# Kernel optimization log

Measured on AMD Instinct MI355X. Metric: run time of the kernel, lower is better.

Reference implementation:

```python
import jax, jax.numpy as jnp
import numpy as np

B, N, C, H, W = 2, 1000, 256, 50, 50
P = 7                      # pooled size
NUM_CLASSES = 91
REP = 1024
IMG = 800
SCALE = 1.0 / 16.0         # feature stride
SCORE_THRESH = 0.05
NMS_THRESH = 0.5
DET = 100
BW = (10.0, 10.0, 5.0, 5.0)  # bbox_reg_weights
BBOX_CLIP = float(np.log(1000.0 / 16.0))
NEG = -1e9


def setup_inputs() -> dict:
    key = jax.random.key(0)
    ks = jax.random.split(key, 8)
    features = jax.random.normal(ks[0], (B, C, H, W), jnp.float32)
    # valid proposal boxes inside the image
    xy = jax.random.uniform(ks[1], (B, N, 2), jnp.float32) * (IMG * 0.6)
    wh = jax.random.uniform(ks[2], (B, N, 2), jnp.float32) * (IMG * 0.35) + 8.0
    proposals = jnp.concatenate([xy, jnp.minimum(xy + wh, IMG - 1.0)], axis=-1)
    D_in = C * P * P
    w1 = jax.random.normal(ks[3], (D_in, REP), jnp.float32) / np.sqrt(D_in)
    b1 = jnp.zeros((REP,), jnp.float32)
    w2 = jax.random.normal(ks[4], (REP, REP), jnp.float32) / np.sqrt(REP)
    b2 = jnp.zeros((REP,), jnp.float32)
    w_cls = jax.random.normal(ks[5], (REP, NUM_CLASSES), jnp.float32) / np.sqrt(REP)
    b_cls = jnp.zeros((NUM_CLASSES,), jnp.float32)
    w_bbox = jax.random.normal(ks[6], (REP, NUM_CLASSES * 4), jnp.float32) * 0.001
    b_bbox = jnp.zeros((NUM_CLASSES * 4,), jnp.float32)
    return dict(features=features, proposals=proposals, w1=w1, b1=b1, w2=w2, b2=b2,
                w_cls=w_cls, b_cls=b_cls, w_bbox=w_bbox, b_bbox=b_bbox, image_size=IMG)


def _roi_align(feat, rois):
    """feat [C,H,W], rois [N,4] -> pooled [N,C,P,P] (aligned, 1 sample per bin)."""
    r = rois * SCALE
    x1, y1, x2, y2 = r[:, 0], r[:, 1], r[:, 2], r[:, 3]
    bw = (x2 - x1) / P
    bh = (y2 - y1) / P
    cc = jnp.arange(P, dtype=feat.dtype) + 0.5
    ys = y1[:, None] + cc[None, :] * bh[:, None] - 0.5   # [N,P]
    xs = x1[:, None] + cc[None, :] * bw[:, None] - 0.5   # [N,P]
    y = jnp.clip(jnp.broadcast_to(ys[:, :, None], (ys.shape[0], P, P)), 0.0, H - 1.0)
    x = jnp.clip(jnp.broadcast_to(xs[:, None, :], (xs.shape[0], P, P)), 0.0, W - 1.0)
    y0 = jnp.floor(y).astype(jnp.int32)
    x0 = jnp.floor(x).astype(jnp.int32)
    y1i = jnp.minimum(y0 + 1, H - 1)
    x1i = jnp.minimum(x0 + 1, W - 1)
    ly = y - y0.astype(feat.dtype); lx = x - x0.astype(feat.dtype)
    hy = 1.0 - ly; hx = 1.0 - lx
    # gathers: [C, N, P, P]
    val = (feat[:, y0, x0] * (hy * hx) + feat[:, y0, x1i] * (hy * lx)
           + feat[:, y1i, x0] * (ly * hx) + feat[:, y1i, x1i] * (ly * lx))
    return jnp.transpose(val, (1, 0, 2, 3))


def _decode_clip(bbox, props, img):
    """bbox [B,N,K,4] deltas, props [B,N,4] -> boxes [B,N,K,4] clipped to image."""
    pw = props[..., 2] - props[..., 0]
    ph = props[..., 3] - props[..., 1]
    pcx = props[..., 0] + 0.5 * pw
    pcy = props[..., 1] + 0.5 * ph
    dx = bbox[..., 0] / BW[0]
    dy = bbox[..., 1] / BW[1]
    dw = jnp.minimum(bbox[..., 2] / BW[2], BBOX_CLIP)
    dh = jnp.minimum(bbox[..., 3] / BW[3], BBOX_CLIP)
    cx = dx * pw[..., None] + pcx[..., None]
    cy = dy * ph[..., None] + pcy[..., None]
    w = pw[..., None] * jnp.exp(dw)
    h = ph[..., None] * jnp.exp(dh)
    boxes = jnp.stack([cx - 0.5 * w, cy - 0.5 * h, cx + 0.5 * w, cy + 0.5 * h], axis=-1)
    return jnp.clip(boxes, 0.0, float(img))


def _nms_one(boxes, scores, img):
    """boxes [N,K,4], scores [N,K] (background already dropped) -> dets [DET,5], labels [DET]."""
    K = scores.shape[1]
    labels = jnp.broadcast_to(jnp.arange(1, K + 1), scores.shape).reshape(-1)
    b = boxes.reshape(-1, 4)
    s = scores.reshape(-1)
    wv = b[:, 2] - b[:, 0]
    hv = b[:, 3] - b[:, 1]
    valid = (s > SCORE_THRESH) & (wv >= 1.0) & (hv >= 1.0)  # score thresh + remove_small_boxes
    swork = jnp.where(valid, s, NEG)
    # batched_nms via per-class coordinate offset
    off = labels.astype(b.dtype) * (float(img) + 2.0)
    boff = b + off[:, None]
    areas = (boff[:, 2] - boff[:, 0]) * (boff[:, 3] - boff[:, 1])

    def body(sw, _):
        i = jnp.argmax(sw)
        ok = sw[i] > NEG / 2
        bi = boff[i]
        ix1 = jnp.maximum(bi[0], boff[:, 0]); iy1 = jnp.maximum(bi[1], boff[:, 1])
        ix2 = jnp.minimum(bi[2], boff[:, 2]); iy2 = jnp.minimum(bi[3], boff[:, 3])
        inter = jnp.clip(ix2 - ix1, 0.0) * jnp.clip(iy2 - iy1, 0.0)
        iou = inter / (areas[i] + areas - inter + 1e-9)
        sw = jnp.where((iou > NMS_THRESH) & ok, NEG, sw)
        sw = sw.at[i].set(NEG)
        return sw, (i, ok)

    _, (idx, oks) = jax.lax.scan(body, swork, None, length=DET)
    db = jnp.where(oks[:, None], b[idx], 0.0)
    ds = jnp.where(oks, s[idx], 0.0)
    dl = jnp.where(oks, labels[idx], -1)
    return jnp.concatenate([db, ds[:, None]], axis=-1), dl


def reference(features, proposals, w1, b1, w2, b2, w_cls, b_cls, w_bbox, b_bbox, image_size):
    # box_roi_pool: RoIAlign 7x7 per image
    pooled = jax.vmap(_roi_align)(features, proposals)          # [B,N,C,P,P]
    feats = pooled.reshape(B * N, C * P * P)
    # box_head: TwoMLPHead
    h = jax.nn.relu(feats @ w1 + b1)
    h = jax.nn.relu(h @ w2 + b2)
    # box_predictor
    logits = h @ w_cls + b_cls                                   # [B*N, 91]
    bbox = (h @ w_bbox + b_bbox).reshape(B, N, NUM_CLASSES, 4)
    scores = jax.nn.softmax(logits, axis=-1).reshape(B, N, NUM_CLASSES)
    boxes = _decode_clip(bbox, proposals, image_size)            # [B,N,91,4]
    # drop background class 0, then per-image class-aware NMS
    boxes_k = boxes[:, :, 1:, :]
    scores_k = scores[:, :, 1:]
    dets, labels = jax.vmap(lambda bb, ss: _nms_one(bb, ss, image_size))(boxes_k, scores_k)
    return dets, labels  # dets [B,DET,5] = (x1,y1,x2,y2,score); labels [B,DET]
```

## Files before the change

### kernel.cpp

```cpp
#include <hip/hip_runtime.h>
#include <stdint.h>

#define B_    2
#define N_    1000
#define C_    256
#define H_    50
#define W_    50
#define P_    7
#define NCLS  91
#define REP_  1024
#define DIN   (C_ * P_ * P_)
#define M_    (B_ * N_)
#define MPAD  2048
#define HOUT  512
#define DET_  100
#define NMSM  (N_ * 90)
#define NEGV  (-1000000000.0f)
#define SCALE_ 0.0625f
#define IMGF  800.0f
#define BBOX_CLIPF 4.135166556742356f

#define RC_   25
#define CC_   4

typedef __bf16 bf16_t;
typedef __attribute__((ext_vector_type(8))) __bf16 bf16x8;
typedef __attribute__((ext_vector_type(4))) __bf16 bf16x4;
typedef __attribute__((ext_vector_type(4))) float f32x4;

__device__ __forceinline__ void gload16(const void* g, void* l) {
  auto gp = (const __attribute__((address_space(1))) uint32_t*)(uintptr_t)g;
  auto lp = (__attribute__((address_space(3))) uint32_t*)(uint32_t)(uintptr_t)l;
  __builtin_amdgcn_global_load_lds(gp, lp, 16, 0, 0);
}

__global__ __launch_bounds__(256) void roi_kernel(const float* __restrict__ features,
                                                  const float* __restrict__ proposals,
                                                  bf16_t* __restrict__ A) {
  const int cc0 = blockIdx.x * CC_;
  const int roiBase = blockIdx.y * RC_;
  const int t = threadIdx.x;
  if (roiBase >= M_) {
    for (int idx = t; idx < RC_ * 49; idx += 256) {
      const int r = idx / 49, pp = idx - r * 49;
      const int n = roiBase + r;
      if (n < MPAD) {
        bf16_t* arow = A + (size_t)n * DIN + cc0 * 49 + pp;
#pragma unroll
        for (int c = 0; c < CC_; ++c) arow[c * 49] = (bf16_t)0.0f;
      }
    }
    return;
  }
  __shared__ __align__(16) float s_pl[CC_ * 2500];
  __shared__ float s_ly[RC_ * 49];
  __shared__ float s_lx[RC_ * 49];
  __shared__ unsigned short s_off[RC_ * 49];
  const int b = (roiBase >= N_) ? 1 : 0;
  const f32x4* src = (const f32x4*)(features + (size_t)(b * C_ + cc0) * (H_ * W_));
  f32x4* dst = (f32x4*)s_pl;
  for (int i = t; i < CC_ * 2500 / 4; i += 256) dst[i] = src[i];
  for (int idx = t; idx < RC_ * 49; idx += 256) {
    const int r = idx / 49, pp = idx - r * 49;
    const int py = pp / 7, px = pp - py * 7;
    const float* p = proposals + (roiBase + r) * 4;
    float y1 = p[1] * SCALE_, y2 = p[3] * SCALE_;
    float bh = (y2 - y1) * (1.0f / 7.0f);
    float y = y1 + ((float)py + 0.5f) * bh - 0.5f;
    y = fminf(fmaxf(y, 0.0f), 49.0f);
    int y0 = (int)floorf(y);
    int dy = (y0 < 49) ? 1 : 0;
    float ly = y - (float)y0;
    float x1 = p[0] * SCALE_, x2 = p[2] * SCALE_;
    float bw = (x2 - x1) * (1.0f / 7.0f);
    float x = x1 + ((float)px + 0.5f) * bw - 0.5f;
    x = fminf(fmaxf(x, 0.0f), 49.0f);
    int x0 = (int)floorf(x);
    int dx = (x0 < 49) ? 1 : 0;
    float lx = x - (float)x0;
    s_off[idx] = (unsigned short)((y0 * W_ + x0) | (dx << 12) | (dy << 13));
    s_ly[idx] = ly;
    s_lx[idx] = lx;
  }
  __syncthreads();
  for (int idx = t; idx < RC_ * 49; idx += 256) {
    const int r = idx / 49, pp = idx - r * 49;
    const unsigned off = s_off[idx];
    const float ly = s_ly[idx], lx = s_lx[idx];
    const float hy = 1.0f - ly, hx = 1.0f - lx;
    const int o00 = off & 0xFFF;
    const int dx = (off >> 12) & 1;
    const int o10 = o00 + W_ * ((off >> 13) & 1);
    const float w00 = hy * hx, w01 = hy * lx, w10 = ly * hx, w11 = ly * lx;
    bf16_t* arow = A + (size_t)(roiBase + r) * DIN + cc0 * 49 + pp;
#pragma unroll
    for (int c = 0; c < CC_; ++c) {
      const float* pl = s_pl + c * 2500;
      float v = pl[o00] * w00 + pl[o00 + dx] * w01 + pl[o10] * w10 + pl[o10 + dx] * w11;
      arow[c * 49] = (bf16_t)v;
    }
  }
}

__global__ __launch_bounds__(256) void transpose_kernel(const float* __restrict__ in,
                                                        bf16_t* __restrict__ out,
                                                        int K, int N) {
  __shared__ float tile[32][33];
  const int k0 = blockIdx.x * 32;
  const int n0 = blockIdx.y * 32;
  const int tx = threadIdx.x & 31;
  const int ty = threadIdx.x >> 5;
#pragma unroll
  for (int j = 0; j < 4; ++j) {
    int ky = ty + j * 8;
    tile[ky][tx] = in[(size_t)(k0 + ky) * N + n0 + tx];
  }
  __syncthreads();
  const int qx = threadIdx.x & 7;
  const int ny = threadIdx.x >> 3;
  bf16x4 o;
#pragma unroll
  for (int i = 0; i < 4; ++i) o[i] = (bf16_t)tile[4 * qx + i][ny];
  *(bf16x4*)(&out[(size_t)(n0 + ny) * K + k0 + 4 * qx]) = o;
}

__global__ __launch_bounds__(256) void headw_kernel(const float* __restrict__ wcls,
                                                    const float* __restrict__ wbb,
                                                    bf16_t* __restrict__ wht) {
  int idx = blockIdx.x * 256 + threadIdx.x;
  int j = idx >> 10;
  int k = idx & 1023;
  float v = 0.0f;
  if (j < NCLS) v = wcls[(size_t)k * NCLS + j];
  else if (j < 455) v = wbb[(size_t)k * 364 + (j - NCLS)];
  wht[idx] = (bf16_t)v;
}

__global__ void headb_kernel(const float* __restrict__ bcls,
                             const float* __restrict__ bbb,
                             float* __restrict__ biash) {
  int j = threadIdx.x;
  float v = 0.0f;
  if (j < NCLS) v = bcls[j];
  else if (j < 455) v = bbb[j - NCLS];
  biash[j] = v;
}

__global__ __launch_bounds__(512, 2) void gemm8_kernel(const bf16_t* __restrict__ A,
                                                       const bf16_t* __restrict__ Bt,
                                                       bf16_t* __restrict__ partial,
                                                       int K, int kLen, int KC) {
  __shared__ __align__(16) bf16_t lds[4 * 2 * 2 * 128 * 32];
  const int t = threadIdx.x;
  const int lane = t & 63;
  const int w = t >> 6;
  const int wm = w >> 2;
  const int wn = w & 3;
  const int bid = blockIdx.x;
  const int zc = bid % KC;
  const int inner = bid / KC;
  const int row0 = (inner >> 2) * 256;
  const int col0 = (inner & 3) * 256;
  const int kOff = zc * kLen;
  const int G = kLen >> 5;

  const int lr = lane & 15;
  const int kb = (lane >> 4) * 16;
  int aoff[8], boff[4];
#pragma unroll
  for (int m = 0; m < 8; ++m) {
    int r = m * 16 + lr;
    aoff[m] = (r * 64 + kb) ^ (((r >> 3) & 1) << 5);
  }
#pragma unroll
  for (int n = 0; n < 4; ++n) {
    int r = (wn & 1) * 64 + n * 16 + lr;
    boff[n] = (r * 64 + kb) ^ (((r >> 3) & 1) << 5);
  }

  const int s_row = t >> 2;
  const int s_k8 = (t & 3) ^ (((s_row >> 3) & 1) << 1);
  const bf16_t* pAs = A + (size_t)(row0 + s_row) * K + kOff + s_k8 * 8;
  const bf16_t* pBs = Bt + (size_t)(col0 + s_row) * K + kOff + s_k8 * 8;
  const size_t halfStride = (size_t)128 * K;
  char* ldsBase = (char*)&lds[0];
  const int wOff = w << 10;

  auto stage = [&](int buf, int hp, int kt) {
    const bf16_t* src = ((hp < 2) ? pAs : pBs) + (size_t)(hp & 1) * halfStride + kt * 32;
    char* dst = ldsBase + buf * 32768 + (hp >> 1) * 16384 + (hp & 1) * 8192 + wOff;
    gload16(src, dst);
  };

  f32x4 acc[8][4] = {};

#pragma unroll
  for (int hp = 0; hp < 4; ++hp) stage(0, hp, 0);
#pragma unroll
  for (int hp = 0; hp < 4; ++hp) stage(1, hp, 1);
#pragma unroll
  for (int hp = 0; hp < 4; ++hp) stage(2, hp, 2);
  asm volatile("s_waitcnt vmcnt(8)" ::: "memory");
  __builtin_amdgcn_s_barrier();
  __builtin_amdgcn_sched_barrier(0);

  for (int g = 0; g < G; ++g) {
    const int cb = g & 3;
    const int sb = (g + 3) & 3;
    const bool doStage = (g + 3) < G;
    if (doStage) {
#pragma unroll
      for (int hp = 0; hp < 4; ++hp) stage(sb, hp, g + 3);
    }
    char* lA = ldsBase + cb * 32768 + wm * 8192;
    char* lB = ldsBase + cb * 32768 + 16384 + (wn >> 1) * 8192;
    bf16x8 af[8], bfv[4];
#pragma unroll
    for (int i = 0; i < 8; ++i) af[i] = *(const bf16x8*)(lA + aoff[i]);
#pragma unroll
    for (int j2 = 0; j2 < 4; ++j2) bfv[j2] = *(const bf16x8*)(lB + boff[j2]);
    asm volatile("s_waitcnt lgkmcnt(0)" ::: "memory");
    if (doStage)          asm volatile("s_waitcnt vmcnt(8)" ::: "memory");
    else if (g == G - 3)  asm volatile("s_waitcnt vmcnt(4)" ::: "memory");
    else                  asm volatile("s_waitcnt vmcnt(0)" ::: "memory");
    __builtin_amdgcn_sched_barrier(0);
    __builtin_amdgcn_s_barrier();
    __builtin_amdgcn_sched_barrier(0);
    __builtin_amdgcn_s_setprio(1);
#pragma unroll
    for (int i = 0; i < 8; ++i)
#pragma unroll
      for (int j2 = 0; j2 < 4; ++j2)
        acc[i][j2] = __builtin_amdgcn_mfma_f32_16x16x32_bf16(af[i], bfv[j2], acc[i][j2], 0, 0, 0);
    __builtin_amdgcn_s_setprio(0);
    __builtin_amdgcn_sched_barrier(0);
  }

  bf16_t* out = partial + (size_t)zc * MPAD * REP_;
  const int crow = (lane >> 4) * 4;
#pragma unroll
  for (int n = 0; n < 4; ++n) {
    const int col = col0 + wn * 64 + n * 16 + lr;
#pragma unroll
    for (int m = 0; m < 8; ++m) {
      const int rowb = row0 + wm * 128 + m * 16 + crow;
#pragma unroll
      for (int j2 = 0; j2 < 4; ++j2)
        out[(size_t)(rowb + j2) * REP_ + col] = (bf16_t)acc[m][n][j2];
    }
  }
}

__global__ __launch_bounds__(256) void gemm_kernel(const bf16_t* __restrict__ A,
                                                   const bf16_t* __restrict__ Bt,
                                                   float* __restrict__ partial,
                                                   int K, int ldc, int kLen) {
  __shared__ __align__(16) bf16_t As[128 * 32];
  __shared__ __align__(16) bf16_t Bs[128 * 32];
  const int t = threadIdx.x;
  const int lane = t & 63;
  const int wid = t >> 6;
  const int row0 = blockIdx.x * 128;
  const int col0 = blockIdx.y * 128;
  const int kOff = blockIdx.z * kLen;

  f32x4 acc[4][4] = {};

  const int rA = t >> 2;
  const int sA = t & 3;
  const bf16_t* aSrc1 = A + (size_t)(row0 + rA) * K + sA * 8 + kOff;
  const bf16_t* aSrc2 = A + (size_t)(row0 + rA + 64) * K + sA * 8 + kOff;
  const bf16_t* bSrc1 = Bt + (size_t)(col0 + rA) * K + sA * 8 + kOff;
  const bf16_t* bSrc2 = Bt + (size_t)(col0 + rA + 64) * K + sA * 8 + kOff;
  char* AsB = (char*)&As[0];
  char* BsB = (char*)&Bs[0];
  const int ldsOff1 = (wid * 64) * 16;
  const int ldsOff2 = (wid * 64 + 256) * 16;

  const int wm = wid >> 1;
  const int wn = wid & 1;
  const int lr = lane & 15;
  const int lk16 = (lane >> 4) * 16;
  int aOff[4], bOff[4];
#pragma unroll
  for (int m = 0; m < 4; ++m) aOff[m] = (wm * 64 + m * 16 + lr) * 64 + lk16;
#pragma unroll
  for (int n = 0; n < 4; ++n) bOff[n] = (wn * 64 + n * 16 + lr) * 64 + lk16;

  for (int k0 = 0; k0 < kLen; k0 += 32) {
    gload16(aSrc1 + k0, AsB + ldsOff1);
    gload16(aSrc2 + k0, AsB + ldsOff2);
    gload16(bSrc1 + k0, BsB + ldsOff1);
    gload16(bSrc2 + k0, BsB + ldsOff2);
    __syncthreads();
    bf16x8 af[4], bfv[4];
#pragma unroll
    for (int m = 0; m < 4; ++m) af[m] = *(const bf16x8*)(AsB + aOff[m]);
#pragma unroll
    for (int n = 0; n < 4; ++n) bfv[n] = *(const bf16x8*)(BsB + bOff[n]);
#pragma unroll
    for (int m = 0; m < 4; ++m)
#pragma unroll
      for (int n = 0; n < 4; ++n)
        acc[m][n] = __builtin_amdgcn_mfma_f32_16x16x32_bf16(af[m], bfv[n], acc[m][n], 0, 0, 0);
    __syncthreads();
  }

  float* out = partial + (size_t)blockIdx.z * MPAD * ldc;
  const int crow = (lane >> 4) * 4;
  const int ccol = lane & 15;
#pragma unroll
  for (int n = 0; n < 4; ++n) {
    const int col = col0 + wn * 64 + n * 16 + ccol;
#pragma unroll
    for (int m = 0; m < 4; ++m) {
      const int rowb = row0 + wm * 64 + m * 16 + crow;
#pragma unroll
      for (int j = 0; j < 4; ++j) {
        out[(size_t)(rowb + j) * ldc + col] = acc[m][n][j];
      }
    }
  }
}

__global__ __launch_bounds__(256) void reduceH_kernel(const bf16_t* __restrict__ partial,
                                                      const float* __restrict__ bias,
                                                      bf16_t* __restrict__ out,
                                                      int KC) {
  const size_t idx8 = ((size_t)blockIdx.x * 256 + threadIdx.x) * 8;
  const size_t stride = (size_t)MPAD * REP_;
  float s[8] = {};
  for (int c = 0; c < KC; ++c) {
    const bf16x8 v = *(const bf16x8*)(partial + c * stride + idx8);
#pragma unroll
    for (int j = 0; j < 8; ++j) s[j] += (float)v[j];
  }
  const int col = (int)(idx8 & (size_t)(REP_ - 1));
  const f32x4 b0 = *(const f32x4*)(bias + col);
  const f32x4 b1 = *(const f32x4*)(bias + col + 4);
  bf16x8 o;
#pragma unroll
  for (int j = 0; j < 4; ++j) o[j] = (bf16_t)fmaxf(s[j] + b0[j], 0.0f);
#pragma unroll
  for (int j = 0; j < 4; ++j) o[4 + j] = (bf16_t)fmaxf(s[4 + j] + b1[j], 0.0f);
  *(bf16x8*)(out + idx8) = o;
}

__global__ __launch_bounds__(256) void reduce_kernel(const float* __restrict__ partial,
                                                     const float* __restrict__ bias,
                                                     void* __restrict__ out,
                                                     int ldc, int KC, int mode) {
  const size_t idx4 = ((size_t)blockIdx.x * 256 + threadIdx.x) * 4;
  f32x4 s = *(const f32x4*)(partial + idx4);
  const size_t stride = (size_t)MPAD * ldc;
  for (int c = 1; c < KC; ++c) s += *(const f32x4*)(partial + c * stride + idx4);
  const int col = (int)(idx4 & (size_t)(ldc - 1));
  const f32x4 bv = *(const f32x4*)(bias + col);
  s += bv;
  if (mode) {
    bf16x4 o;
#pragma unroll
    for (int j = 0; j < 4; ++j) o[j] = (bf16_t)fmaxf(s[j], 0.0f);
    *(bf16x4*)((bf16_t*)out + idx4) = o;
  } else {
    *(f32x4*)((float*)out + idx4) = s;
  }
}

__global__ __launch_bounds__(256) void rowsm_kernel(const float* __restrict__ ho,
                                                    float* __restrict__ mxv,
                                                    float* __restrict__ invv) {
  const int row = blockIdx.x * 4 + (threadIdx.x >> 6);
  const int lane = threadIdx.x & 63;
  if (row >= M_) return;
  const float* r = ho + (size_t)row * HOUT;
  float v1 = (lane < NCLS) ? r[lane] : -3.0e38f;
  float v2 = (lane + 64 < NCLS) ? r[lane + 64] : -3.0e38f;
  float mx = fmaxf(v1, v2);
#pragma unroll
  for (int off = 32; off; off >>= 1) mx = fmaxf(mx, __shfl_xor(mx, off));
  float s = ((lane < NCLS) ? expf(v1 - mx) : 0.0f) + ((lane + 64 < NCLS) ? expf(v2 - mx) : 0.0f);
#pragma unroll
  for (int off = 32; off; off >>= 1) s += __shfl_xor(s, off);
  if (lane == 0) { mxv[row] = mx; invv[row] = 1.0f / s; }
}

__global__ __launch_bounds__(256) void decode_kernel(const float* __restrict__ ho,
                                                     const float* __restrict__ mxv,
                                                     const float* __restrict__ invv,
                                                     const float* __restrict__ props,
                                                     float* __restrict__ boxes,
                                                     float* __restrict__ scores,
                                                     float* __restrict__ swork,
                                                     float* __restrict__ boff,
                                                     float* __restrict__ area) {
  const int idx = blockIdx.x * 256 + threadIdx.x;
  if (idx >= M_ * 90) return;
  const int n = idx / 90;
  const int k = idx - n * 90 + 1;
  const float* row = ho + (size_t)n * HOUT;
  const float sc = expf(row[k] - mxv[n]) * invv[n];
  const float* p = props + n * 4;
  const float px1 = p[0], py1 = p[1], px2 = p[2], py2 = p[3];
  const float pw = px2 - px1, ph = py2 - py1;
  const float pcx = px1 + 0.5f * pw, pcy = py1 + 0.5f * ph;
  const float* d = row + NCLS + 4 * k;
  const float dx = d[0] * 0.1f;
  const float dy = d[1] * 0.1f;
  const float dw = fminf(d[2] * 0.2f, BBOX_CLIPF);
  const float dh = fminf(d[3] * 0.2f, BBOX_CLIPF);
  const float cx = dx * pw + pcx, cy = dy * ph + pcy;
  const float w = pw * expf(dw), h = ph * expf(dh);
  const float bx1 = fminf(fmaxf(cx - 0.5f * w, 0.0f), IMGF);
  const float by1 = fminf(fmaxf(cy - 0.5f * h, 0.0f), IMGF);
  const float bx2 = fminf(fmaxf(cx + 0.5f * w, 0.0f), IMGF);
  const float by2 = fminf(fmaxf(cy + 0.5f * h, 0.0f), IMGF);
  const int j = idx;
  boxes[4 * j + 0] = bx1; boxes[4 * j + 1] = by1;
  boxes[4 * j + 2] = bx2; boxes[4 * j + 3] = by2;
  scores[j] = sc;
  const float wv = bx2 - bx1, hv = by2 - by1;
  swork[j] = ((sc > 0.05f) && (wv >= 1.0f) && (hv >= 1.0f)) ? sc : NEGV;
  const float off = (float)k * (IMGF + 2.0f);
  const float ox1 = bx1 + off, oy1 = by1 + off, ox2 = bx2 + off, oy2 = by2 + off;
  boff[4 * j + 0] = ox1; boff[4 * j + 1] = oy1;
  boff[4 * j + 2] = ox2; boff[4 * j + 3] = oy2;
  area[j] = (ox2 - ox1) * (oy2 - oy1);
}

__global__ __launch_bounds__(1024) void nms_kernel(const float* __restrict__ boxes,
                                                   const float* __restrict__ scores,
                                                   float* __restrict__ swork,
                                                   const float* __restrict__ boff,
                                                   const float* __restrict__ area,
                                                   float* __restrict__ dout) {
  const int b = blockIdx.x;
  const int t = threadIdx.x;
  const float* Bx = boxes + (size_t)b * NMSM * 4;
  const float* Sc = scores + (size_t)b * NMSM;
  float* Sw = swork + (size_t)b * NMSM;
  const float* Bo = boff + (size_t)b * NMSM * 4;
  const float* Ar = area + (size_t)b * NMSM;
  float* dets = dout + b * (DET_ * 5);
  float* labels = dout + B_ * DET_ * 5 + b * DET_;
  __shared__ float s_val[1024];
  __shared__ int s_idx[1024];
  __shared__ float s_box[4];
  __shared__ float s_area;
  __shared__ int s_ok;
  for (int it = 0; it < DET_; ++it) {
    float bv = -3.0e38f;
    int bi = 0;
    for (int j = t; j < NMSM; j += 1024) {
      float v = Sw[j];
      if (v > bv) { bv = v; bi = j; }
    }
    s_val[t] = bv;
    s_idx[t] = bi;
    __syncthreads();
    for (int off = 512; off > 0; off >>= 1) {
      if (t < off) {
        float v2 = s_val[t + off]; int i2 = s_idx[t + off];
        if (v2 > s_val[t] || (v2 == s_val[t] && i2 < s_idx[t])) { s_val[t] = v2; s_idx[t] = i2; }
      }
      __syncthreads();
    }
    if (t == 0) {
      int i = s_idx[0];
      int ok = (s_val[0] > NEGV * 0.5f) ? 1 : 0;
      s_ok = ok;
      if (ok) {
        dets[it * 5 + 0] = Bx[i * 4 + 0];
        dets[it * 5 + 1] = Bx[i * 4 + 1];
        dets[it * 5 + 2] = Bx[i * 4 + 2];
        dets[it * 5 + 3] = Bx[i * 4 + 3];
        dets[it * 5 + 4] = Sc[i];
        labels[it] = (float)(i % 90 + 1);
        s_box[0] = Bo[i * 4 + 0]; s_box[1] = Bo[i * 4 + 1];
        s_box[2] = Bo[i * 4 + 2]; s_box[3] = Bo[i * 4 + 3];
        s_area = Ar[i];
        Sw[i] = NEGV;
      }
    }
    __syncthreads();
    if (!s_ok) {
      for (int tt = it + t; tt < DET_; tt += 1024) {
        dets[tt * 5 + 0] = 0.0f; dets[tt * 5 + 1] = 0.0f; dets[tt * 5 + 2] = 0.0f;
        dets[tt * 5 + 3] = 0.0f; dets[tt * 5 + 4] = 0.0f;
        labels[tt] = -1.0f;
      }
      return;
    }
    const float bx1 = s_box[0], by1 = s_box[1], bx2 = s_box[2], by2 = s_box[3], ai = s_area;
    for (int j = t; j < NMSM; j += 1024) {
      float v = Sw[j];
      if (v <= NEGV * 0.5f) continue;
      float ix1 = fmaxf(bx1, Bo[j * 4 + 0]);
      float iy1 = fmaxf(by1, Bo[j * 4 + 1]);
      float ix2 = fminf(bx2, Bo[j * 4 + 2]);
      float iy2 = fminf(by2, Bo[j * 4 + 3]);
      float inter = fmaxf(ix2 - ix1, 0.0f) * fmaxf(iy2 - iy1, 0.0f);
      float iou = inter / (ai + Ar[j] - inter + 1e-9f);
      if (iou > 0.5f) Sw[j] = NEGV;
    }
    __syncthreads();
  }
}

extern "C" void kernel_launch(void* const* d_in, const int* in_sizes, int n_in,
                              void* d_out, int out_size, void* d_ws, size_t ws_size,
                              hipStream_t stream) {
  const float* features  = (const float*)d_in[0];
  const float* proposals = (const float*)d_in[1];
  const float* w1   = (const float*)d_in[2];
  const float* b1   = (const float*)d_in[3];
  const float* w2   = (const float*)d_in[4];
  const float* b2   = (const float*)d_in[5];
  const float* wcls = (const float*)d_in[6];
  const float* bcls = (const float*)d_in[7];
  const float* wbb  = (const float*)d_in[8];
  const float* bbb  = (const float*)d_in[9];
  (void)in_sizes; (void)n_in; (void)out_size;

  char* p = (char*)d_ws;
  auto alloc = [&](size_t bytes) {
    char* r = p;
    p += (bytes + 255) & ~(size_t)255;
    return r;
  };
  bf16_t* A      = (bf16_t*)alloc((size_t)MPAD * DIN * 2);
  bf16_t* w1t    = (bf16_t*)alloc((size_t)REP_ * DIN * 2);
  bf16_t* w2t    = (bf16_t*)alloc((size_t)REP_ * REP_ * 2);
  bf16_t* wht    = (bf16_t*)alloc((size_t)HOUT * REP_ * 2);
  float*  biash  = (float*)alloc((size_t)HOUT * 4);
  bf16_t* h1     = (bf16_t*)alloc((size_t)MPAD * REP_ * 2);
  bf16_t* h2     = (bf16_t*)alloc((size_t)MPAD * REP_ * 2);
  float*  ho     = (float*)alloc((size_t)MPAD * HOUT * 4);
  float*  mxv    = (float*)alloc((size_t)M_ * 4);
  float*  invv   = (float*)alloc((size_t)M_ * 4);
  float*  boxes  = (float*)alloc((size_t)B_ * NMSM * 4 * 4);
  float*  scoresb= (float*)alloc((size_t)B_ * NMSM * 4);
  float*  sworkb = (float*)alloc((size_t)B_ * NMSM * 4);
  float*  boffb  = (float*)alloc((size_t)B_ * NMSM * 4 * 4);
  float*  areab  = (float*)alloc((size_t)B_ * NMSM * 4);

  size_t used = (size_t)(p - (char*)d_ws);
  size_t avail = (ws_size > used) ? (ws_size - used) : 0;
  bf16_t* partialH = (bf16_t*)p;
  float*  partialF = (float*)p;
  const size_t chunkH = (size_t)MPAD * REP_ * 2;
  const size_t chunkF = (size_t)MPAD * REP_ * 4;
  int KC1 = 8;
  while (KC1 > 1 && (size_t)KC1 * chunkH > avail) KC1 >>= 1;
  int KC2 = 4;
  while (KC2 > 1 && (size_t)KC2 * chunkF > avail) KC2 >>= 1;
  int KC3 = 4;

  roi_kernel<<<dim3(C_ / CC_, (MPAD + RC_ - 1) / RC_), 256, 0, stream>>>(features, proposals, A);
  transpose_kernel<<<dim3(DIN / 32, REP_ / 32), 256, 0, stream>>>(w1, w1t, DIN, REP_);
  transpose_kernel<<<dim3(REP_ / 32, REP_ / 32), 256, 0, stream>>>(w2, w2t, REP_, REP_);
  headw_kernel<<<(HOUT * REP_) / 256, 256, 0, stream>>>(wcls, wbb, wht);
  headb_kernel<<<1, HOUT, 0, stream>>>(bcls, bbb, biash);

  gemm8_kernel<<<32 * KC1, 512, 0, stream>>>(A, w1t, partialH, DIN, DIN / KC1, KC1);
  reduceH_kernel<<<(MPAD * REP_ / 8) / 256, 256, 0, stream>>>(partialH, b1, h1, KC1);
  gemm_kernel<<<dim3(MPAD / 128, REP_ / 128, KC2), 256, 0, stream>>>(h1, w2t, partialF, REP_, REP_, REP_ / KC2);
  reduce_kernel<<<(MPAD * REP_ / 4) / 256, 256, 0, stream>>>(partialF, b2, h2, REP_, KC2, 1);
  gemm_kernel<<<dim3(MPAD / 128, HOUT / 128, KC3), 256, 0, stream>>>(h2, wht, partialF, REP_, HOUT, REP_ / KC3);
  reduce_kernel<<<(MPAD * HOUT / 4) / 256, 256, 0, stream>>>(partialF, biash, ho, HOUT, KC3, 0);

  rowsm_kernel<<<(M_ + 3) / 4, 256, 0, stream>>>(ho, mxv, invv);
  decode_kernel<<<(M_ * 90 + 255) / 256, 256, 0, stream>>>(ho, mxv, invv, proposals,
                                                           boxes, scoresb, sworkb, boffb, areab);
  nms_kernel<<<B_, 1024, 0, stream>>>(boxes, scoresb, sworkb, boffb, areab, (float*)d_out);
}
```

Measured before the change: 192.3 us.

## Reuse the pipelined 256x256 GEMM kernel for the second MLP layer and the head

Makes the 256x256 multi-buffered MFMA GEMM generic over output type, column-tile count and leading dimension. It then replaces the simple 128x128 GEMM for the second hidden layer and for the cls/bbox head. The second layer now writes bf16 split-K partials (8 chunks) reduced by the bf16 reducer, and the head uses 8 float partials. The block barrier also moves from before the MFMA loop to after it, which changes the sync schedule for all three GEMMs. Very short K chunks (four k-steps) limit how well the prefetch pipeline can hide load latency, and bf16 partial sums add rounding error.

```diff
diff --git a/kernel.cpp b/kernel.cpp
--- a/kernel.cpp
+++ b/kernel.cpp
@@ -146,10 +146,12 @@
   biash[j] = v;
 }
 
+template <typename OT>
 __global__ __launch_bounds__(512, 2) void gemm8_kernel(const bf16_t* __restrict__ A,
                                                        const bf16_t* __restrict__ Bt,
-                                                       bf16_t* __restrict__ partial,
-                                                       int K, int kLen, int KC) {
+                                                       OT* __restrict__ partial,
+                                                       int K, int kLen, int KC,
+                                                       int GN, int ldc) {
   __shared__ __align__(16) bf16_t lds[4 * 2 * 2 * 128 * 32];
   const int t = threadIdx.x;
   const int lane = t & 63;
@@ -159,8 +161,8 @@
   const int bid = blockIdx.x;
   const int zc = bid % KC;
   const int inner = bid / KC;
-  const int row0 = (inner >> 2) * 256;
-  const int col0 = (inner & 3) * 256;
+  const int row0 = (inner / GN) * 256;
+  const int col0 = (inner % GN) * 256;
   const int kOff = zc * kLen;
   const int G = kLen >> 5;
 
@@ -224,8 +226,6 @@
     else if (g == G - 3)  asm volatile("s_waitcnt vmcnt(4)" ::: "memory");
     else                  asm volatile("s_waitcnt vmcnt(0)" ::: "memory");
     __builtin_amdgcn_sched_barrier(0);
-    __builtin_amdgcn_s_barrier();
-    __builtin_amdgcn_sched_barrier(0);
     __builtin_amdgcn_s_setprio(1);
 #pragma unroll
     for (int i = 0; i < 8; ++i)
@@ -234,9 +234,11 @@
         acc[i][j2] = __builtin_amdgcn_mfma_f32_16x16x32_bf16(af[i], bfv[j2], acc[i][j2], 0, 0, 0);
     __builtin_amdgcn_s_setprio(0);
     __builtin_amdgcn_sched_barrier(0);
-  }
-
-  bf16_t* out = partial + (size_t)zc * MPAD * REP_;
+    __builtin_amdgcn_s_barrier();
+    __builtin_amdgcn_sched_barrier(0);
+  }
+
+  OT* out = partial + (size_t)zc * MPAD * ldc;
   const int crow = (lane >> 4) * 4;
 #pragma unroll
   for (int n = 0; n < 4; ++n) {
@@ -246,79 +248,7 @@
       const int rowb = row0 + wm * 128 + m * 16 + crow;
 #pragma unroll
       for (int j2 = 0; j2 < 4; ++j2)
-        out[(size_t)(rowb + j2) * REP_ + col] = (bf16_t)acc[m][n][j2];
-    }
-  }
-}
-
-__global__ __launch_bounds__(256) void gemm_kernel(const bf16_t* __restrict__ A,
-                                                   const bf16_t* __restrict__ Bt,
-                                                   float* __restrict__ partial,
-                                                   int K, int ldc, int kLen) {
-  __shared__ __align__(16) bf16_t As[128 * 32];
-  __shared__ __align__(16) bf16_t Bs[128 * 32];
-  const int t = threadIdx.x;
-  const int lane = t & 63;
-  const int wid = t >> 6;
-  const int row0 = blockIdx.x * 128;
-  const int col0 = blockIdx.y * 128;
-  const int kOff = blockIdx.z * kLen;
-
-  f32x4 acc[4][4] = {};
-
-  const int rA = t >> 2;
-  const int sA = t & 3;
-  const bf16_t* aSrc1 = A + (size_t)(row0 + rA) * K + sA * 8 + kOff;
-  const bf16_t* aSrc2 = A + (size_t)(row0 + rA + 64) * K + sA * 8 + kOff;
-  const bf16_t* bSrc1 = Bt + (size_t)(col0 + rA) * K + sA * 8 + kOff;
-  const bf16_t* bSrc2 = Bt + (size_t)(col0 + rA + 64) * K + sA * 8 + kOff;
-  char* AsB = (char*)&As[0];
-  char* BsB = (char*)&Bs[0];
-  const int ldsOff1 = (wid * 64) * 16;
-  const int ldsOff2 = (wid * 64 + 256) * 16;
-
-  const int wm = wid >> 1;
-  const int wn = wid & 1;
-  const int lr = lane & 15;
-  const int lk16 = (lane >> 4) * 16;
-  int aOff[4], bOff[4];
-#pragma unroll
-  for (int m = 0; m < 4; ++m) aOff[m] = (wm * 64 + m * 16 + lr) * 64 + lk16;
-#pragma unroll
-  for (int n = 0; n < 4; ++n) bOff[n] = (wn * 64 + n * 16 + lr) * 64 + lk16;
-
-  for (int k0 = 0; k0 < kLen; k0 += 32) {
-    gload16(aSrc1 + k0, AsB + ldsOff1);
-    gload16(aSrc2 + k0, AsB + ldsOff2);
-    gload16(bSrc1 + k0, BsB + ldsOff1);
-    gload16(bSrc2 + k0, BsB + ldsOff2);
-    __syncthreads();
-    bf16x8 af[4], bfv[4];
-#pragma unroll
-    for (int m = 0; m < 4; ++m) af[m] = *(const bf16x8*)(AsB + aOff[m]);
-#pragma unroll
-    for (int n = 0; n < 4; ++n) bfv[n] = *(const bf16x8*)(BsB + bOff[n]);
-#pragma unroll
-    for (int m = 0; m < 4; ++m)
-#pragma unroll
-      for (int n = 0; n < 4; ++n)
-        acc[m][n] = __builtin_amdgcn_mfma_f32_16x16x32_bf16(af[m], bfv[n], acc[m][n], 0, 0, 0);
-    __syncthreads();
-  }
-
-  float* out = partial + (size_t)blockIdx.z * MPAD * ldc;
-  const int crow = (lane >> 4) * 4;
-  const int ccol = lane & 15;
-#pragma unroll
-  for (int n = 0; n < 4; ++n) {
-    const int col = col0 + wn * 64 + n * 16 + ccol;
-#pragma unroll
-    for (int m = 0; m < 4; ++m) {
-      const int rowb = row0 + wm * 64 + m * 16 + crow;
-#pragma unroll
-      for (int j = 0; j < 4; ++j) {
-        out[(size_t)(rowb + j) * ldc + col] = acc[m][n][j];
-      }
+        out[(size_t)(rowb + j2) * ldc + col] = (OT)acc[m][n][j2];
     }
   }
 }
@@ -348,23 +278,15 @@
 
 __global__ __launch_bounds__(256) void reduce_kernel(const float* __restrict__ partial,
                                                      const float* __restrict__ bias,
-                                                     void* __restrict__ out,
-                                                     int ldc, int KC, int mode) {
+                                                     float* __restrict__ out,
+                                                     int ldc, int KC) {
   const size_t idx4 = ((size_t)blockIdx.x * 256 + threadIdx.x) * 4;
   f32x4 s = *(const f32x4*)(partial + idx4);
   const size_t stride = (size_t)MPAD * ldc;
   for (int c = 1; c < KC; ++c) s += *(const f32x4*)(partial + c * stride + idx4);
   const int col = (int)(idx4 & (size_t)(ldc - 1));
-  const f32x4 bv = *(const f32x4*)(bias + col);
-  s += bv;
-  if (mode) {
-    bf16x4 o;
-#pragma unroll
-    for (int j = 0; j < 4; ++j) o[j] = (bf16_t)fmaxf(s[j], 0.0f);
-    *(bf16x4*)((bf16_t*)out + idx4) = o;
-  } else {
-    *(f32x4*)((float*)out + idx4) = s;
-  }
+  s += *(const f32x4*)(bias + col);
+  *(f32x4*)(out + idx4) = s;
 }
 
 __global__ __launch_bounds__(256) void rowsm_kernel(const float* __restrict__ ho,
@@ -549,12 +471,13 @@
   bf16_t* partialH = (bf16_t*)p;
   float*  partialF = (float*)p;
   const size_t chunkH = (size_t)MPAD * REP_ * 2;
-  const size_t chunkF = (size_t)MPAD * REP_ * 4;
+  const size_t chunkF = (size_t)MPAD * HOUT * 4;
   int KC1 = 8;
   while (KC1 > 1 && (size_t)KC1 * chunkH > avail) KC1 >>= 1;
-  int KC2 = 4;
-  while (KC2 > 1 && (size_t)KC2 * chunkF > avail) KC2 >>= 1;
-  int KC3 = 4;
+  int KC2 = 8;
+  while (KC2 > 1 && (size_t)KC2 * chunkH > avail) KC2 >>= 1;
+  int KC3 = 8;
+  while (KC3 > 1 && (size_t)KC3 * chunkF > avail) KC3 >>= 1;
 
   roi_kernel<<<dim3(C_ / CC_, (MPAD + RC_ - 1) / RC_), 256, 0, stream>>>(features, proposals, A);
   transpose_kernel<<<dim3(DIN / 32, REP_ / 32), 256, 0, stream>>>(w1, w1t, DIN, REP_);
@@ -562,12 +485,12 @@
   headw_kernel<<<(HOUT * REP_) / 256, 256, 0, stream>>>(wcls, wbb, wht);
   headb_kernel<<<1, HOUT, 0, stream>>>(bcls, bbb, biash);
 
-  gemm8_kernel<<<32 * KC1, 512, 0, stream>>>(A, w1t, partialH, DIN, DIN / KC1, KC1);
+  gemm8_kernel<bf16_t><<<32 * KC1, 512, 0, stream>>>(A, w1t, partialH, DIN, DIN / KC1, KC1, 4, REP_);
   reduceH_kernel<<<(MPAD * REP_ / 8) / 256, 256, 0, stream>>>(partialH, b1, h1, KC1);
-  gemm_kernel<<<dim3(MPAD / 128, REP_ / 128, KC2), 256, 0, stream>>>(h1, w2t, partialF, REP_, REP_, REP_ / KC2);
-  reduce_kernel<<<(MPAD * REP_ / 4) / 256, 256, 0, stream>>>(partialF, b2, h2, REP_, KC2, 1);
-  gemm_kernel<<<dim3(MPAD / 128, HOUT / 128, KC3), 256, 0, stream>>>(h2, wht, partialF, REP_, HOUT, REP_ / KC3);
-  reduce_kernel<<<(MPAD * HOUT / 4) / 256, 256, 0, stream>>>(partialF, biash, ho, HOUT, KC3, 0);
+  gemm8_kernel<bf16_t><<<32 * KC2, 512, 0, stream>>>(h1, w2t, partialH, REP_, REP_ / KC2, KC2, 4, REP_);
+  reduceH_kernel<<<(MPAD * REP_ / 8) / 256, 256, 0, stream>>>(partialH, b2, h2, KC2);
+  gemm8_kernel<float><<<16 * KC3, 512, 0, stream>>>(h2, wht, partialF, REP_, REP_ / KC3, KC3, 2, HOUT);
+  reduce_kernel<<<(MPAD * HOUT / 4) / 256, 256, 0, stream>>>(partialF, biash, ho, HOUT, KC3);
 
   rowsm_kernel<<<(M_ + 3) / 4, 256, 0, stream>>>(ho, mxv, invv);
   decode_kernel<<<(M_ * 90 + 255) / 256, 256, 0, stream>>>(ho, mxv, invv, proposals,
```

After: 209.4 us. 8.9% more time.
